# Performance work log

Measured on AMD Instinct MI355X. Metric: run time of the kernel, lower is better.

The kernel has to match this reference:

```python
import jax, jax.numpy as jnp
import numpy as np

DIM = 384
HEADS = 6
N_TOKEN = 2240
HIDDEN = int(DIM * 4.0)
EPS = 1e-5


def layernorm(x, g, b):
    mu = jnp.mean(x, axis=-1, keepdims=True)
    var = jnp.mean(jnp.square(x - mu), axis=-1, keepdims=True)
    return (x - mu) * jax.lax.rsqrt(var + EPS) * g + b


def setup_inputs() -> dict:
    key = jax.random.key(0)
    ks = jax.random.split(key, 10)
    B, N, C = 2, 2240, DIM
    s = 0.02
    return {
        "x": jax.random.normal(ks[0], (B, N, C), dtype=jnp.float32),
        "encoder_pos": jax.random.normal(ks[1], (1, N_TOKEN, C), dtype=jnp.float32) * s,
        "ln1_g": jnp.ones((C,), jnp.float32),
        "ln1_b": jnp.zeros((C,), jnp.float32),
        "w_qkv": jax.random.normal(ks[2], (3 * C, C), dtype=jnp.float32) * s,  # torch Linear [out,in], no bias
        "w_proj": jax.random.normal(ks[3], (C, C), dtype=jnp.float32) * s,
        "b_proj": jnp.zeros((C,), jnp.float32),
        "ln2_g": jnp.ones((C,), jnp.float32),
        "ln2_b": jnp.zeros((C,), jnp.float32),
        "w_fc1": jax.random.normal(ks[4], (HIDDEN, C), dtype=jnp.float32) * s,
        "b_fc1": jnp.zeros((HIDDEN,), jnp.float32),
        "w_fc2": jax.random.normal(ks[5], (C, HIDDEN), dtype=jnp.float32) * s,
        "b_fc2": jnp.zeros((C,), jnp.float32),
    }


def reference(x, encoder_pos, ln1_g, ln1_b, w_qkv, w_proj, b_proj, ln2_g, ln2_b, w_fc1, b_fc1, w_fc2, b_fc2):
    B, N, C = x.shape
    H = HEADS
    hd = C // H
    scale = hd ** -0.5

    # positional embedding: each of the n_token rows repeated N//n_token times (contiguously)
    rep = N // encoder_pos.shape[1]
    pos = jnp.repeat(encoder_pos, rep, axis=1)  # [1, N, C]
    x = x + pos

    # attention
    h = layernorm(x, ln1_g, ln1_b)
    qkv = h @ w_qkv.T  # [B, N, 3C]
    qkv = qkv.reshape(B, N, 3, H, hd).transpose(2, 0, 3, 1, 4)  # [3, B, H, N, hd]
    q, k, v = qkv[0], qkv[1], qkv[2]
    attn = jax.nn.softmax(jnp.einsum("bhqd,bhkd->bhqk", q, k) * scale, axis=-1)  # [B, H, N, N]
    o = jnp.einsum("bhqk,bhkd->bhqd", attn, v).transpose(0, 2, 1, 3).reshape(B, N, C)
    o = o @ w_proj.T + b_proj
    x = x + o

    # MLP
    h = layernorm(x, ln2_g, ln2_b)
    h = jax.nn.gelu(h @ w_fc1.T + b_fc1, approximate=False)
    h = h @ w_fc2.T + b_fc2
    x = x + h
    return (x, attn)
```

## Files before the change

### kernel.cpp

```cpp
#include <hip/hip_runtime.h>
#include <math.h>

typedef unsigned short u16;
typedef unsigned int   u32;
typedef __attribute__((ext_vector_type(8))) short short8;
typedef __attribute__((ext_vector_type(4))) float floatx4;

#define MFMA16(a,b,c) __builtin_amdgcn_mfma_f32_16x16x32_bf16((a),(b),(c),0,0,0)

constexpr int BB  = 2;
constexpr int NT  = 2240;
constexpr int CD  = 384;
constexpr int NH  = 6;
constexpr int HD  = 64;
constexpr int HID = 1536;
constexpr int M   = BB * NT;
constexpr int CS  = 5;
constexpr int CTILES = NT / 64 / CS;
constexpr float SCALE = 0.125f;

__device__ inline u16 f2bf(float f) {
  u32 u = __float_as_uint(f);
  u = (u + 0x7fffu + ((u >> 16) & 1u)) >> 16;
  return (u16)u;
}
__device__ inline float bf2f(u16 b) { return __uint_as_float(((u32)b) << 16); }

__device__ inline uint4 sum5_bf(uint4 a0, uint4 a1, uint4 a2, uint4 a3, uint4 a4) {
  union U { uint4 v; u16 h[8]; };
  U u0, u1, u2, u3, u4, o;
  u0.v = a0; u1.v = a1; u2.v = a2; u3.v = a3; u4.v = a4;
  #pragma unroll
  for (int e = 0; e < 8; ++e) {
    float f = bf2f(u0.h[e]) + bf2f(u1.h[e]) + bf2f(u2.h[e]) + bf2f(u3.h[e]) + bf2f(u4.h[e]);
    o.h[e] = f2bf(f);
  }
  return o.v;
}

constexpr int NQ = 3 * CD * CD, NP = CD * CD, N1 = HID * CD, N2 = CD * HID;
constexpr int CVT_BLOCKS = (NQ + NP + N1 + N2) / 512;

__global__ __launch_bounds__(128) void ln_cvt_kernel(
    const float* __restrict__ xin, const float* __restrict__ pos,
    const float* __restrict__ g, const float* __restrict__ bta,
    float* __restrict__ x1out, u16* __restrict__ hout,
    const float* __restrict__ s0, u16* __restrict__ d0,
    const float* __restrict__ s1, u16* __restrict__ d1,
    const float* __restrict__ s2, u16* __restrict__ d2,
    const float* __restrict__ s3, u16* __restrict__ d3) {
  int t = threadIdx.x;
  if (blockIdx.x >= M) {
    int i = ((blockIdx.x - M) * 128 + t) * 4;
    const float* s; u16* d; int base;
    if (i < NQ)                { s = s0; d = d0; base = 0; }
    else if (i < NQ + NP)      { s = s1; d = d1; base = NQ; }
    else if (i < NQ + NP + N1) { s = s2; d = d2; base = NQ + NP; }
    else                       { s = s3; d = d3; base = NQ + NP + N1; }
    int j = i - base;
    float4 v = *(const float4*)(s + j);
    ushort4 o; o.x = f2bf(v.x); o.y = f2bf(v.y); o.z = f2bf(v.z); o.w = f2bf(v.w);
    *(ushort4*)(d + j) = o;
    return;
  }
  int row = blockIdx.x;
  int n = row % NT;
  const float* xr = xin + (size_t)row * CD;
  float v[3], s1v = 0.f, s2v = 0.f;
  #pragma unroll
  for (int j = 0; j < 3; ++j) {
    int c = t + j * 128;
    float x = xr[c] + pos[(size_t)n * CD + c];
    v[j] = x; s1v += x; s2v += x * x;
  }
  #pragma unroll
  for (int off = 32; off; off >>= 1) { s1v += __shfl_down(s1v, off); s2v += __shfl_down(s2v, off); }
  __shared__ float rbuf[4];
  __shared__ float stats[2];
  int lane = t & 63, wid = t >> 6;
  if (lane == 0) { rbuf[wid] = s1v; rbuf[2 + wid] = s2v; }
  __syncthreads();
  if (t == 0) {
    float a = rbuf[0] + rbuf[1], b2 = rbuf[2] + rbuf[3];
    float mu = a / CD;
    float var = b2 / CD - mu * mu;
    stats[0] = mu; stats[1] = rsqrtf(var + 1e-5f);
  }
  __syncthreads();
  float mu = stats[0], rs = stats[1];
  #pragma unroll
  for (int j = 0; j < 3; ++j) {
    int c = t + j * 128;
    float h = (v[j] - mu) * rs * g[c] + bta[c];
    hout[(size_t)row * CD + c] = f2bf(h);
    x1out[(size_t)row * CD + c] = v[j];
  }
}

__global__ __launch_bounds__(128) void ln_kernel(
    const float* __restrict__ xin,
    const float* __restrict__ g, const float* __restrict__ bta,
    u16* __restrict__ hout) {
  int row = blockIdx.x;
  int t = threadIdx.x;
  const float* xr = xin + (size_t)row * CD;
  float v[3], s1 = 0.f, s2 = 0.f;
  #pragma unroll
  for (int j = 0; j < 3; ++j) {
    int c = t + j * 128;
    float x = xr[c];
    v[j] = x; s1 += x; s2 += x * x;
  }
  #pragma unroll
  for (int off = 32; off; off >>= 1) { s1 += __shfl_down(s1, off); s2 += __shfl_down(s2, off); }
  __shared__ float rbuf[4];
  __shared__ float stats[2];
  int lane = t & 63, wid = t >> 6;
  if (lane == 0) { rbuf[wid] = s1; rbuf[2 + wid] = s2; }
  __syncthreads();
  if (t == 0) {
    float a = rbuf[0] + rbuf[1], b2 = rbuf[2] + rbuf[3];
    float mu = a / CD;
    float var = b2 / CD - mu * mu;
    stats[0] = mu; stats[1] = rsqrtf(var + 1e-5f);
  }
  __syncthreads();
  float mu = stats[0], rs = stats[1];
  #pragma unroll
  for (int j = 0; j < 3; ++j) {
    int c = t + j * 128;
    hout[(size_t)row * CD + c] = f2bf((v[j] - mu) * rs * g[c] + bta[c]);
  }
}

template <int EPI, bool OSUM>
__global__ __launch_bounds__(256) void gemm_bt(
    const u16* __restrict__ A, const u16* __restrict__ Wt, int K,
    const float* __restrict__ bias, const float* __restrict__ res,
    float* __restrict__ outf, u16* __restrict__ outb,
    u16* __restrict__ qout, u16* __restrict__ kout, u16* __restrict__ vtout) {
  __shared__ __align__(16) u16 As[64][72];
  __shared__ __align__(16) u16 Bs[64][72];
  int m0 = blockIdx.y * 64, n0 = blockIdx.x * 64;
  int t = threadIdx.x;
  int lane = t & 63, w = t >> 6, wm = w & 1, wn = w >> 1;
  int quad = lane >> 4, c16 = lane & 15;
  int lrow = t >> 2, lseg = t & 3;
  constexpr int SL = OSUM ? 5 : 1;
  const u16* ga[SL];
  #pragma unroll
  for (int s = 0; s < SL; ++s)
    ga[s] = A + (size_t)s * M * CD + (size_t)(m0 + lrow) * K + lseg * 8;
  const u16* gb = Wt + (size_t)(n0 + lrow) * K + lseg * 8;
  floatx4 acc[2][2] = {};
  uint4 av0[SL], av1[SL], bv0, bv1;
  #pragma unroll
  for (int s = 0; s < SL; ++s) { av0[s] = *(const uint4*)(ga[s]); av1[s] = *(const uint4*)(ga[s] + 32); }
  bv0 = *(const uint4*)(gb);
  bv1 = *(const uint4*)(gb + 32);
  for (int k0 = 0; k0 < K; k0 += 64) {
    __syncthreads();
    uint4 wa0, wa1;
    if (OSUM) {
      wa0 = sum5_bf(av0[0], av0[1], av0[2], av0[3], av0[4 % SL]);
      wa1 = sum5_bf(av1[0], av1[1], av1[2], av1[3], av1[4 % SL]);
    } else { wa0 = av0[0]; wa1 = av1[0]; }
    *(uint4*)&As[lrow][lseg * 8] = wa0;
    *(uint4*)&As[lrow][32 + lseg * 8] = wa1;
    *(uint4*)&Bs[lrow][lseg * 8] = bv0;
    *(uint4*)&Bs[lrow][32 + lseg * 8] = bv1;
    __syncthreads();
    if (k0 + 64 < K) {
      #pragma unroll
      for (int s = 0; s < SL; ++s) {
        av0[s] = *(const uint4*)(ga[s] + k0 + 64);
        av1[s] = *(const uint4*)(ga[s] + k0 + 96);
      }
      bv0 = *(const uint4*)(gb + k0 + 64);
      bv1 = *(const uint4*)(gb + k0 + 96);
    }
    #pragma unroll
    for (int ks = 0; ks < 2; ++ks) {
      short8 af[2], bf[2];
      #pragma unroll
      for (int mt = 0; mt < 2; ++mt) af[mt] = *(const short8*)&As[wm * 32 + mt * 16 + c16][ks * 32 + quad * 8];
      #pragma unroll
      for (int nt = 0; nt < 2; ++nt) bf[nt] = *(const short8*)&Bs[wn * 32 + nt * 16 + c16][ks * 32 + quad * 8];
      #pragma unroll
      for (int mt = 0; mt < 2; ++mt)
        #pragma unroll
        for (int nt = 0; nt < 2; ++nt)
          acc[mt][nt] = MFMA16(af[mt], bf[nt], acc[mt][nt]);
    }
  }
  if (EPI == 0) {
    int s = n0 / 384;
    int hh = (n0 % 384) / 64;
    int b_ = m0 / NT, nn0 = m0 % NT;
    __syncthreads();
    #pragma unroll
    for (int mt = 0; mt < 2; ++mt)
      #pragma unroll
      for (int nt = 0; nt < 2; ++nt)
        #pragma unroll
        for (int r = 0; r < 4; ++r) {
          int m_l = wm * 32 + mt * 16 + quad * 4 + r;
          int d_l = wn * 32 + nt * 16 + c16;
          u16 bv = f2bf(acc[mt][nt][r]);
          if (s < 2) As[m_l][d_l] = bv;
          else       As[d_l][m_l] = bv;
        }
    __syncthreads();
    int row = t >> 2, cs0 = (t & 3) * 16;
    uint4 va = *(const uint4*)&As[row][cs0];
    uint4 vb = *(const uint4*)&As[row][cs0 + 8];
    u16* dst;
    if (s == 0)      dst = qout  + ((size_t)(b_ * NH + hh) * NT + nn0 + row) * HD + cs0;
    else if (s == 1) dst = kout  + ((size_t)(b_ * NH + hh) * NT + nn0 + row) * HD + cs0;
    else             dst = vtout + ((size_t)(b_ * NH + hh) * HD + row) * NT + nn0 + cs0;
    *(uint4*)dst = va;
    *(uint4*)(dst + 8) = vb;
  } else {
    #pragma unroll
    for (int mt = 0; mt < 2; ++mt) {
      #pragma unroll
      for (int nt = 0; nt < 2; ++nt) {
        int rg0 = m0 + wm * 32 + mt * 16 + quad * 4;
        int cg = n0 + wn * 32 + nt * 16 + c16;
        #pragma unroll
        for (int r = 0; r < 4; ++r) {
          float v = acc[mt][nt][r];
          int m = rg0 + r;
          if (EPI == 2) {
            v += bias[cg];
            v = 0.5f * v * (1.0f + erff(v * 0.70710678118f));
            outb[(size_t)m * HID + cg] = f2bf(v);
          } else {
            outf[(size_t)m * CD + cg] = v + bias[cg] + res[(size_t)m * CD + cg];
          }
        }
      }
    }
  }
}

__global__ __launch_bounds__(256) void attn_pass1(
    const u16* __restrict__ qb, const u16* __restrict__ kb, float* __restrict__ ml) {
  __shared__ __align__(16) u16 Ks[64][72];
  int bh = blockIdx.y, chunk = blockIdx.z;
  int q0 = blockIdx.x * 64;
  int t = threadIdx.x, w = t >> 6, lane = t & 63, quad = lane >> 4, c16 = lane & 15;
  int lrow = t >> 2, lseg = t & 3;

  const u16* qp = qb + ((size_t)bh * NT + q0 + w * 16 + c16) * HD;
  short8 qf0 = *(const short8*)(qp + quad * 8);
  short8 qf1 = *(const short8*)(qp + 32 + quad * 8);
  const u16* kbase = kb + (size_t)bh * NT * HD;

  float m_i = -1e30f, l_i = 0.f;

  const u16* kg = kbase + (size_t)(chunk * CTILES * 64 + lrow) * HD + lseg * 8;
  uint4 kv0 = *(const uint4*)kg;
  uint4 kv1 = *(const uint4*)(kg + 32);

  for (int ct = 0; ct < CTILES; ++ct) {
    __syncthreads();
    *(uint4*)&Ks[lrow][lseg * 8] = kv0;
    *(uint4*)&Ks[lrow][32 + lseg * 8] = kv1;
    __syncthreads();
    if (ct + 1 < CTILES) {
      const u16* kn = kbase + (size_t)((chunk * CTILES + ct + 1) * 64 + lrow) * HD + lseg * 8;
      kv0 = *(const uint4*)kn;
      kv1 = *(const uint4*)(kn + 32);
    }
    floatx4 s_acc[4] = {};
    #pragma unroll
    for (int nt = 0; nt < 4; ++nt) {
      const u16* kp = &Ks[nt * 16 + c16][quad * 8];
      s_acc[nt] = MFMA16(*(const short8*)(kp), qf0, s_acc[nt]);
      s_acc[nt] = MFMA16(*(const short8*)(kp + 32), qf1, s_acc[nt]);
    }
    float rm = -1e30f;
    #pragma unroll
    for (int nt = 0; nt < 4; ++nt)
      #pragma unroll
      for (int r = 0; r < 4; ++r) rm = fmaxf(rm, s_acc[nt][r]);
    rm *= SCALE;
    rm = fmaxf(rm, __shfl_xor(rm, 16));
    rm = fmaxf(rm, __shfl_xor(rm, 32));
    float nm = fmaxf(m_i, rm);
    float ps = 0.f;
    #pragma unroll
    for (int nt = 0; nt < 4; ++nt)
      #pragma unroll
      for (int r = 0; r < 4; ++r) ps += __expf(s_acc[nt][r] * SCALE - nm);
    ps += __shfl_xor(ps, 16);
    ps += __shfl_xor(ps, 32);
    l_i = l_i * __expf(m_i - nm) + ps;
    m_i = nm;
  }
  if (quad == 0) {
    int row = q0 + w * 16 + c16;
    float* p = ml + ((size_t)(bh * NT + row) * CS + chunk) * 2;
    p[0] = m_i; p[1] = l_i;
  }
}

__global__ __launch_bounds__(256) void attn_pass2(
    const u16* __restrict__ qb, const u16* __restrict__ kb, const u16* __restrict__ vtb,
    const float* __restrict__ ml, float* __restrict__ attn_out, u16* __restrict__ o_part) {
  __shared__ __align__(16) u16 Ks[64][72];
  __shared__ __align__(16) u16 Vs[64][72];
  __shared__ __align__(16) u16 Plds[4][16][72];
  __shared__ float mfin[64], rlfin[64];
  int bh = blockIdx.y, chunk = blockIdx.z;
  int b = bh / NH, hh = bh % NH;
  int q0 = blockIdx.x * 64;
  int t = threadIdx.x, w = t >> 6, lane = t & 63, quad = lane >> 4, c16 = lane & 15;
  int lrow = t >> 2, lseg = t & 3;

  const u16* kbase = kb + (size_t)bh * NT * HD;
  const u16* vbase = vtb + (size_t)bh * HD * NT;

  int col00 = chunk * CTILES * 64;
  const u16* kg = kbase + (size_t)(col00 + lrow) * HD + lseg * 8;
  const u16* vg = vbase + (size_t)lrow * NT + col00 + lseg * 8;
  uint4 kv0 = *(const uint4*)kg;
  uint4 kv1 = *(const uint4*)(kg + 32);
  uint4 vv0 = *(const uint4*)vg;
  uint4 vv1 = *(const uint4*)(vg + 32);

  if (t < 64) {
    const float* p = ml + (size_t)(bh * NT + q0 + t) * CS * 2;
    float mm = -1e30f;
    #pragma unroll
    for (int c = 0; c < CS; ++c) mm = fmaxf(mm, p[c * 2]);
    float ll = 0.f;
    #pragma unroll
    for (int c = 0; c < CS; ++c) ll += p[c * 2 + 1] * __expf(p[c * 2] - mm);
    mfin[t] = mm; rlfin[t] = 1.0f / ll;
  }
  __syncthreads();
  float m_i[4], rl[4];
  #pragma unroll
  for (int r = 0; r < 4; ++r) {
    int rr = w * 16 + quad * 4 + r;
    m_i[r] = mfin[rr]; rl[r] = rlfin[rr];
  }

  const u16* qp = qb + ((size_t)bh * NT + q0 + w * 16 + c16) * HD;
  short8 qf0 = *(const short8*)(qp + quad * 8);
  short8 qf1 = *(const short8*)(qp + 32 + quad * 8);

  floatx4 o_acc[4] = {};
  float* attn_bh = attn_out + (size_t)bh * NT * NT;
  for (int ct = 0; ct < CTILES; ++ct) {
    int col0 = (chunk * CTILES + ct) * 64;
    __syncthreads();
    *(uint4*)&Ks[lrow][lseg * 8] = kv0;
    *(uint4*)&Ks[lrow][32 + lseg * 8] = kv1;
    *(uint4*)&Vs[lrow][lseg * 8] = vv0;
    *(uint4*)&Vs[lrow][32 + lseg * 8] = vv1;
    __syncthreads();
    if (ct + 1 < CTILES) {
      int coln = col0 + 64;
      const u16* kn = kbase + (size_t)(coln + lrow) * HD + lseg * 8;
      const u16* vn = vbase + (size_t)lrow * NT + coln + lseg * 8;
      kv0 = *(const uint4*)kn;
      kv1 = *(const uint4*)(kn + 32);
      vv0 = *(const uint4*)vn;
      vv1 = *(const uint4*)(vn + 32);
    }
    floatx4 s_acc[4] = {};
    #pragma unroll
    for (int nt = 0; nt < 4; ++nt) {
      const u16* kp = &Ks[nt * 16 + c16][quad * 8];
      s_acc[nt] = MFMA16(qf0, *(const short8*)(kp), s_acc[nt]);
      s_acc[nt] = MFMA16(qf1, *(const short8*)(kp + 32), s_acc[nt]);
    }
    #pragma unroll
    for (int nt = 0; nt < 4; ++nt) {
      #pragma unroll
      for (int r = 0; r < 4; ++r) {
        float p = __expf(s_acc[nt][r] * SCALE - m_i[r]) * rl[r];
        __builtin_nontemporal_store(
            p, &attn_bh[(size_t)(q0 + w * 16 + quad * 4 + r) * NT + col0 + nt * 16 + c16]);
        Plds[w][quad * 4 + r][nt * 16 + c16] = f2bf(p);
      }
    }
    #pragma unroll
    for (int ks = 0; ks < 2; ++ks) {
      short8 pa = *(const short8*)&Plds[w][c16][ks * 32 + quad * 8];
      #pragma unroll
      for (int dt = 0; dt < 4; ++dt) {
        short8 vb = *(const short8*)&Vs[dt * 16 + c16][ks * 32 + quad * 8];
        o_acc[dt] = MFMA16(pa, vb, o_acc[dt]);
      }
    }
  }
  #pragma unroll
  for (int dt = 0; dt < 4; ++dt) {
    #pragma unroll
    for (int r = 0; r < 4; ++r) {
      int m = b * NT + q0 + w * 16 + quad * 4 + r;
      int cc = hh * 64 + dt * 16 + c16;
      o_part[((size_t)chunk * M + m) * CD + cc] = f2bf(o_acc[dt][r]);
    }
  }
}

extern "C" void kernel_launch(void* const* d_in, const int* in_sizes, int n_in,
                              void* d_out, int out_size, void* d_ws, size_t ws_size,
                              hipStream_t stream) {
  const float* x      = (const float*)d_in[0];
  const float* pos    = (const float*)d_in[1];
  const float* ln1_g  = (const float*)d_in[2];
  const float* ln1_b  = (const float*)d_in[3];
  const float* w_qkv  = (const float*)d_in[4];
  const float* w_proj = (const float*)d_in[5];
  const float* b_proj = (const float*)d_in[6];
  const float* ln2_g  = (const float*)d_in[7];
  const float* ln2_b  = (const float*)d_in[8];
  const float* w_fc1  = (const float*)d_in[9];
  const float* b_fc1  = (const float*)d_in[10];
  const float* w_fc2  = (const float*)d_in[11];
  const float* b_fc2  = (const float*)d_in[12];

  float* out      = (float*)d_out;
  float* attn_out = out + (size_t)M * CD;

  char* ws = (char*)d_ws;
  size_t o = 0;
  auto carve = [&](size_t bytes) { char* p = ws + o; o += bytes; return p; };
  float* x1    = (float*)carve((size_t)M * CD * 4);
  u16* h1      = (u16*)carve((size_t)M * CD * 2);
  u16* wqkv_b  = (u16*)carve((size_t)3 * CD * CD * 2);
  u16* wproj_b = (u16*)carve((size_t)CD * CD * 2);
  u16* wfc1_b  = (u16*)carve((size_t)HID * CD * 2);
  u16* wfc2_b  = (u16*)carve((size_t)CD * HID * 2);
  u16* q_bf    = (u16*)carve((size_t)BB * NH * NT * HD * 2);
  u16* k_bf    = (u16*)carve((size_t)BB * NH * NT * HD * 2);
  u16* vt_bf   = (u16*)carve((size_t)BB * NH * NT * HD * 2);
  float* x2    = (float*)carve((size_t)M * CD * 4);
  u16* h2      = (u16*)carve((size_t)M * CD * 2);
  u16* g_bf    = (u16*)carve((size_t)M * HID * 2);
  float* ml    = (float*)carve((size_t)NH * BB * NT * CS * 2 * 4);
  u16* o_part  = (u16*)carve((size_t)CS * M * CD * 2);
  (void)ws_size; (void)in_sizes; (void)n_in; (void)out_size;

  ln_cvt_kernel<<<M + CVT_BLOCKS, 128, 0, stream>>>(
      x, pos, ln1_g, ln1_b, x1, h1,
      w_qkv, wqkv_b, w_proj, wproj_b, w_fc1, wfc1_b, w_fc2, wfc2_b);

  gemm_bt<0, false><<<dim3((3 * CD) / 64, M / 64), 256, 0, stream>>>(
      h1, wqkv_b, CD, nullptr, nullptr, nullptr, nullptr, q_bf, k_bf, vt_bf);

  attn_pass1<<<dim3(NT / 64, BB * NH, CS), 256, 0, stream>>>(q_bf, k_bf, ml);
  attn_pass2<<<dim3(NT / 64, BB * NH, CS), 256, 0, stream>>>(q_bf, k_bf, vt_bf, ml, attn_out, o_part);

  gemm_bt<3, true><<<dim3(CD / 64, M / 64), 256, 0, stream>>>(
      o_part, wproj_b, CD, b_proj, x1, x2, nullptr, nullptr, nullptr, nullptr);
  ln_kernel<<<M, 128, 0, stream>>>(x2, ln2_g, ln2_b, h2);

  gemm_bt<2, false><<<dim3(HID / 64, M / 64), 256, 0, stream>>>(
      h2, wfc1_b, CD, b_fc1, nullptr, nullptr, g_bf, nullptr, nullptr, nullptr);

  gemm_bt<3, false><<<dim3(CD / 64, M / 64), 256, 0, stream>>>(
      g_bf, wfc2_b, HID, b_fc2, x2, out, nullptr, nullptr, nullptr, nullptr);
}
```

Measured before the change: 410.8 us.

## Fuse LayerNorm2 into FC1 GEMM and use direct global-to-LDS loads with swizzle

Removes the standalone LN2 kernel and the h2 buffer. The FC1 GEMM now computes per-row mean and rstd from fp32 x2 itself and normalizes on the fly while staging A into LDS. Weight tiles, and A tiles for plain bf16 inputs, are loaded with global_load_lds straight into unpadded LDS, which uses an XOR swizzle to avoid bank conflicts. This cuts one launch, one intermediate round trip and register staging. In exchange, every N-column block of FC1 recomputes the row statistics, and the direct loads lose the previous register prefetch overlap.

```diff
diff --git a/kernel.cpp b/kernel.cpp
--- a/kernel.cpp
+++ b/kernel.cpp
@@ -25,6 +25,12 @@
   return (u16)u;
 }
 __device__ inline float bf2f(u16 b) { return __uint_as_float(((u32)b) << 16); }
+
+__device__ inline void gload16(const u16* g, u16* l) {
+  __builtin_amdgcn_global_load_lds(
+      (const __attribute__((address_space(1))) u32*)g,
+      (__attribute__((address_space(3))) u32*)l, 16, 0, 0);
+}
 
 __device__ inline uint4 sum5_bf(uint4 a0, uint4 a1, uint4 a2, uint4 a3, uint4 a4) {
   union U { uint4 v; u16 h[8]; };
@@ -97,95 +103,132 @@
   }
 }
 
-__global__ __launch_bounds__(128) void ln_kernel(
-    const float* __restrict__ xin,
-    const float* __restrict__ g, const float* __restrict__ bta,
-    u16* __restrict__ hout) {
-  int row = blockIdx.x;
-  int t = threadIdx.x;
-  const float* xr = xin + (size_t)row * CD;
-  float v[3], s1 = 0.f, s2 = 0.f;
-  #pragma unroll
-  for (int j = 0; j < 3; ++j) {
-    int c = t + j * 128;
-    float x = xr[c];
-    v[j] = x; s1 += x; s2 += x * x;
-  }
-  #pragma unroll
-  for (int off = 32; off; off >>= 1) { s1 += __shfl_down(s1, off); s2 += __shfl_down(s2, off); }
-  __shared__ float rbuf[4];
-  __shared__ float stats[2];
-  int lane = t & 63, wid = t >> 6;
-  if (lane == 0) { rbuf[wid] = s1; rbuf[2 + wid] = s2; }
-  __syncthreads();
-  if (t == 0) {
-    float a = rbuf[0] + rbuf[1], b2 = rbuf[2] + rbuf[3];
-    float mu = a / CD;
-    float var = b2 / CD - mu * mu;
-    stats[0] = mu; stats[1] = rsqrtf(var + 1e-5f);
-  }
-  __syncthreads();
-  float mu = stats[0], rs = stats[1];
-  #pragma unroll
-  for (int j = 0; j < 3; ++j) {
-    int c = t + j * 128;
-    hout[(size_t)row * CD + c] = f2bf((v[j] - mu) * rs * g[c] + bta[c]);
-  }
-}
-
-template <int EPI, bool OSUM>
+template <int EPI, int AMODE>
 __global__ __launch_bounds__(256) void gemm_bt(
-    const u16* __restrict__ A, const u16* __restrict__ Wt, int K,
+    const u16* __restrict__ A, const float* __restrict__ Af,
+    const u16* __restrict__ Wt, int K,
     const float* __restrict__ bias, const float* __restrict__ res,
+    const float* __restrict__ lng, const float* __restrict__ lnb,
     float* __restrict__ outf, u16* __restrict__ outb,
     u16* __restrict__ qout, u16* __restrict__ kout, u16* __restrict__ vtout) {
-  __shared__ __align__(16) u16 As[64][72];
-  __shared__ __align__(16) u16 Bs[64][72];
+  __shared__ __align__(16) u16 As[64][64];
+  __shared__ __align__(16) u16 Bs[64][64];
+  __shared__ float mu_s[64], rs_s[64];
   int m0 = blockIdx.y * 64, n0 = blockIdx.x * 64;
   int t = threadIdx.x;
   int lane = t & 63, w = t >> 6, wm = w & 1, wn = w >> 1;
   int quad = lane >> 4, c16 = lane & 15;
   int lrow = t >> 2, lseg = t & 3;
-  constexpr int SL = OSUM ? 5 : 1;
+  int l8 = lane >> 3;
+  int colsel = ((lane & 7) ^ l8) * 8;
+  int r7 = c16 & 7;
+
+  const u16* gbsrc = Wt + (size_t)(n0 + w * 16 + l8) * K + colsel;
+  u16* ldsB = &Bs[w * 16][0];
+  const u16* gasrc = nullptr; u16* ldsA = nullptr;
+  if constexpr (AMODE == 0) {
+    gasrc = A + (size_t)(m0 + w * 16 + l8) * K + colsel;
+    ldsA = &As[w * 16][0];
+  }
+
+  if constexpr (AMODE == 2) {
+    const float* xr = Af + (size_t)(m0 + lrow) * CD + lseg * 96;
+    float s1 = 0.f, s2 = 0.f;
+    #pragma unroll
+    for (int j2 = 0; j2 < 24; ++j2) {
+      float4 v = *(const float4*)(xr + j2 * 4);
+      s1 += v.x + v.y + v.z + v.w;
+      s2 += v.x * v.x + v.y * v.y + v.z * v.z + v.w * v.w;
+    }
+    s1 += __shfl_xor(s1, 1); s2 += __shfl_xor(s2, 1);
+    s1 += __shfl_xor(s1, 2); s2 += __shfl_xor(s2, 2);
+    if (lseg == 0) {
+      float mu = s1 / CD, var = s2 / CD - mu * mu;
+      mu_s[lrow] = mu; rs_s[lrow] = rsqrtf(var + 1e-5f);
+    }
+  }
+
+  constexpr int SL = (AMODE == 1) ? 5 : 1;
   const u16* ga[SL];
-  #pragma unroll
-  for (int s = 0; s < SL; ++s)
-    ga[s] = A + (size_t)s * M * CD + (size_t)(m0 + lrow) * K + lseg * 8;
-  const u16* gb = Wt + (size_t)(n0 + lrow) * K + lseg * 8;
+  uint4 av0[SL], av1[SL];
+  float4 lf0, lf1, lf2, lf3;
+  if constexpr (AMODE == 1) {
+    #pragma unroll
+    for (int s = 0; s < SL; ++s) {
+      ga[s] = A + (size_t)s * M * CD + (size_t)(m0 + lrow) * CD + lseg * 8;
+      av0[s] = *(const uint4*)(ga[s]);
+      av1[s] = *(const uint4*)(ga[s] + 32);
+    }
+  } else if constexpr (AMODE == 2) {
+    const float* ar = Af + (size_t)(m0 + lrow) * CD + lseg * 8;
+    lf0 = *(const float4*)(ar);      lf1 = *(const float4*)(ar + 4);
+    lf2 = *(const float4*)(ar + 32); lf3 = *(const float4*)(ar + 36);
+  }
+
   floatx4 acc[2][2] = {};
-  uint4 av0[SL], av1[SL], bv0, bv1;
-  #pragma unroll
-  for (int s = 0; s < SL; ++s) { av0[s] = *(const uint4*)(ga[s]); av1[s] = *(const uint4*)(ga[s] + 32); }
-  bv0 = *(const uint4*)(gb);
-  bv1 = *(const uint4*)(gb + 32);
   for (int k0 = 0; k0 < K; k0 += 64) {
     __syncthreads();
-    uint4 wa0, wa1;
-    if (OSUM) {
-      wa0 = sum5_bf(av0[0], av0[1], av0[2], av0[3], av0[4 % SL]);
-      wa1 = sum5_bf(av1[0], av1[1], av1[2], av1[3], av1[4 % SL]);
-    } else { wa0 = av0[0]; wa1 = av1[0]; }
-    *(uint4*)&As[lrow][lseg * 8] = wa0;
-    *(uint4*)&As[lrow][32 + lseg * 8] = wa1;
-    *(uint4*)&Bs[lrow][lseg * 8] = bv0;
-    *(uint4*)&Bs[lrow][32 + lseg * 8] = bv1;
+    #pragma unroll
+    for (int j = 0; j < 2; ++j) {
+      gload16(gbsrc + (size_t)j * 8 * K + k0, ldsB + j * 512);
+      if constexpr (AMODE == 0)
+        gload16(gasrc + (size_t)j * 8 * K + k0, ldsA + j * 512);
+    }
+    if constexpr (AMODE == 1) {
+      uint4 wa0 = sum5_bf(av0[0], av0[1], av0[2], av0[3], av0[4]);
+      uint4 wa1 = sum5_bf(av1[0], av1[1], av1[2], av1[3], av1[4]);
+      *(uint4*)&As[lrow][(lseg ^ (lrow & 7)) * 8] = wa0;
+      *(uint4*)&As[lrow][((4 + lseg) ^ (lrow & 7)) * 8] = wa1;
+    } else if constexpr (AMODE == 2) {
+      float mu = mu_s[lrow], rs = rs_s[lrow];
+      union { uint4 v; u16 h[8]; } pk;
+      int cb = k0 + lseg * 8;
+      float4 g0 = *(const float4*)(lng + cb), g1 = *(const float4*)(lng + cb + 4);
+      float4 b0 = *(const float4*)(lnb + cb), b1 = *(const float4*)(lnb + cb + 4);
+      pk.h[0] = f2bf((lf0.x - mu) * rs * g0.x + b0.x);
+      pk.h[1] = f2bf((lf0.y - mu) * rs * g0.y + b0.y);
+      pk.h[2] = f2bf((lf0.z - mu) * rs * g0.z + b0.z);
+      pk.h[3] = f2bf((lf0.w - mu) * rs * g0.w + b0.w);
+      pk.h[4] = f2bf((lf1.x - mu) * rs * g1.x + b1.x);
+      pk.h[5] = f2bf((lf1.y - mu) * rs * g1.y + b1.y);
+      pk.h[6] = f2bf((lf1.z - mu) * rs * g1.z + b1.z);
+      pk.h[7] = f2bf((lf1.w - mu) * rs * g1.w + b1.w);
+      *(uint4*)&As[lrow][(lseg ^ (lrow & 7)) * 8] = pk.v;
+      int cb2 = cb + 32;
+      float4 g2 = *(const float4*)(lng + cb2), g3 = *(const float4*)(lng + cb2 + 4);
+      float4 b2 = *(const float4*)(lnb + cb2), b3 = *(const float4*)(lnb + cb2 + 4);
+      pk.h[0] = f2bf((lf2.x - mu) * rs * g2.x + b2.x);
+      pk.h[1] = f2bf((lf2.y - mu) * rs * g2.y + b2.y);
+      pk.h[2] = f2bf((lf2.z - mu) * rs * g2.z + b2.z);
+      pk.h[3] = f2bf((lf2.w - mu) * rs * g2.w + b2.w);
+      pk.h[4] = f2bf((lf3.x - mu) * rs * g3.x + b3.x);
+      pk.h[5] = f2bf((lf3.y - mu) * rs * g3.y + b3.y);
+      pk.h[6] = f2bf((lf3.z - mu) * rs * g3.z + b3.z);
+      pk.h[7] = f2bf((lf3.w - mu) * rs * g3.w + b3.w);
+      *(uint4*)&As[lrow][((4 + lseg) ^ (lrow & 7)) * 8] = pk.v;
+    }
     __syncthreads();
     if (k0 + 64 < K) {
-      #pragma unroll
-      for (int s = 0; s < SL; ++s) {
-        av0[s] = *(const uint4*)(ga[s] + k0 + 64);
-        av1[s] = *(const uint4*)(ga[s] + k0 + 96);
+      if constexpr (AMODE == 1) {
+        #pragma unroll
+        for (int s = 0; s < SL; ++s) {
+          av0[s] = *(const uint4*)(ga[s] + k0 + 64);
+          av1[s] = *(const uint4*)(ga[s] + k0 + 96);
+        }
+      } else if constexpr (AMODE == 2) {
+        const float* ar = Af + (size_t)(m0 + lrow) * CD + k0 + 64 + lseg * 8;
+        lf0 = *(const float4*)(ar);      lf1 = *(const float4*)(ar + 4);
+        lf2 = *(const float4*)(ar + 32); lf3 = *(const float4*)(ar + 36);
       }
-      bv0 = *(const uint4*)(gb + k0 + 64);
-      bv1 = *(const uint4*)(gb + k0 + 96);
     }
     #pragma unroll
     for (int ks = 0; ks < 2; ++ks) {
+      int cswz = ((ks * 4 + quad) ^ r7) * 8;
       short8 af[2], bf[2];
       #pragma unroll
-      for (int mt = 0; mt < 2; ++mt) af[mt] = *(const short8*)&As[wm * 32 + mt * 16 + c16][ks * 32 + quad * 8];
-      #pragma unroll
-      for (int nt = 0; nt < 2; ++nt) bf[nt] = *(const short8*)&Bs[wn * 32 + nt * 16 + c16][ks * 32 + quad * 8];
+      for (int mt = 0; mt < 2; ++mt) af[mt] = *(const short8*)&As[wm * 32 + mt * 16 + c16][cswz];
+      #pragma unroll
+      for (int nt = 0; nt < 2; ++nt) bf[nt] = *(const short8*)&Bs[wn * 32 + nt * 16 + c16][cswz];
       #pragma unroll
       for (int mt = 0; mt < 2; ++mt)
         #pragma unroll
@@ -193,7 +236,7 @@
           acc[mt][nt] = MFMA16(af[mt], bf[nt], acc[mt][nt]);
     }
   }
-  if (EPI == 0) {
+  if constexpr (EPI == 0) {
     int s = n0 / 384;
     int hh = (n0 % 384) / 64;
     int b_ = m0 / NT, nn0 = m0 % NT;
@@ -207,13 +250,14 @@
           int m_l = wm * 32 + mt * 16 + quad * 4 + r;
           int d_l = wn * 32 + nt * 16 + c16;
           u16 bv = f2bf(acc[mt][nt][r]);
-          if (s < 2) As[m_l][d_l] = bv;
-          else       As[d_l][m_l] = bv;
+          if (s < 2) As[m_l][d_l ^ ((m_l & 7) << 3)] = bv;
+          else       As[d_l][m_l ^ ((d_l & 7) << 3)] = bv;
         }
     __syncthreads();
-    int row = t >> 2, cs0 = (t & 3) * 16;
-    uint4 va = *(const uint4*)&As[row][cs0];
-    uint4 vb = *(const uint4*)&As[row][cs0 + 8];
+    int row = t >> 2, q2 = (t & 3) * 2;
+    uint4 va = *(const uint4*)&As[row][(q2 ^ (row & 7)) * 8];
+    uint4 vb = *(const uint4*)&As[row][((q2 + 1) ^ (row & 7)) * 8];
+    int cs0 = (t & 3) * 16;
     u16* dst;
     if (s == 0)      dst = qout  + ((size_t)(b_ * NH + hh) * NT + nn0 + row) * HD + cs0;
     else if (s == 1) dst = kout  + ((size_t)(b_ * NH + hh) * NT + nn0 + row) * HD + cs0;
@@ -231,7 +275,7 @@
         for (int r = 0; r < 4; ++r) {
           float v = acc[mt][nt][r];
           int m = rg0 + r;
-          if (EPI == 2) {
+          if constexpr (EPI == 2) {
             v += bias[cg];
             v = 0.5f * v * (1.0f + erff(v * 0.70710678118f));
             outb[(size_t)m * HID + cg] = f2bf(v);
@@ -442,7 +486,6 @@
   u16* k_bf    = (u16*)carve((size_t)BB * NH * NT * HD * 2);
   u16* vt_bf   = (u16*)carve((size_t)BB * NH * NT * HD * 2);
   float* x2    = (float*)carve((size_t)M * CD * 4);
-  u16* h2      = (u16*)carve((size_t)M * CD * 2);
   u16* g_bf    = (u16*)carve((size_t)M * HID * 2);
   float* ml    = (float*)carve((size_t)NH * BB * NT * CS * 2 * 4);
   u16* o_part  = (u16*)carve((size_t)CS * M * CD * 2);
@@ -452,19 +495,22 @@
       x, pos, ln1_g, ln1_b, x1, h1,
       w_qkv, wqkv_b, w_proj, wproj_b, w_fc1, wfc1_b, w_fc2, wfc2_b);
 
-  gemm_bt<0, false><<<dim3((3 * CD) / 64, M / 64), 256, 0, stream>>>(
-      h1, wqkv_b, CD, nullptr, nullptr, nullptr, nullptr, q_bf, k_bf, vt_bf);
+  gemm_bt<0, 0><<<dim3((3 * CD) / 64, M / 64), 256, 0, stream>>>(
+      h1, nullptr, wqkv_b, CD, nullptr, nullptr, nullptr, nullptr,
+      nullptr, nullptr, q_bf, k_bf, vt_bf);
 
   attn_pass1<<<dim3(NT / 64, BB * NH, CS), 256, 0, stream>>>(q_bf, k_bf, ml);
   attn_pass2<<<dim3(NT / 64, BB * NH, CS), 256, 0, stream>>>(q_bf, k_bf, vt_bf, ml, attn_out, o_part);
 
-  gemm_bt<3, true><<<dim3(CD / 64, M / 64), 256, 0, stream>>>(
-      o_part, wproj_b, CD, b_proj, x1, x2, nullptr, nullptr, nullptr, nullptr);
-  ln_kernel<<<M, 128, 0, stream>>>(x2, ln2_g, ln2_b, h2);
-
-  gemm_bt<2, false><<<dim3(HID / 64, M / 64), 256, 0, stream>>>(
-      h2, wfc1_b, CD, b_fc1, nullptr, nullptr, g_bf, nullptr, nullptr, nullptr);
-
-  gemm_bt<3, false><<<dim3(CD / 64, M / 64), 256, 0, stream>>>(
-      g_bf, wfc2_b, HID, b_fc2, x2, out, nullptr, nullptr, nullptr, nullptr);
-}
+  gemm_bt<3, 1><<<dim3(CD / 64, M / 64), 256, 0, stream>>>(
+      o_part, nullptr, wproj_b, CD, b_proj, x1, nullptr, nullptr,
+      x2, nullptr, nullptr, nullptr, nullptr);
+
+  gemm_bt<2, 2><<<dim3(HID / 64, M / 64), 256, 0, stream>>>(
+      nullptr, x2, wfc1_b, CD, b_fc1, nullptr, ln2_g, ln2_b,
+      nullptr, g_bf, nullptr, nullptr, nullptr);
+
+  gemm_bt<3, 0><<<dim3(CD / 64, M / 64), 256, 0, stream>>>(
+      g_bf, nullptr, wfc2_b, HID, b_fc2, x2, nullptr, nullptr,
+      out, nullptr, nullptr, nullptr, nullptr);
+}
```

Result: slower. 432.8 us (+5.4%).
